# Kernel tuning notes

Measured on AMD Instinct MI355X. Metric: run time of the kernel, lower is better.

The kernel has to match this reference:

```python
import jax, jax.numpy as jnp
import numpy as np

N_ROIS = 10000
N_CLS = 151          # Visual Genome: 150 object classes + background
NMS_THRESH = 0.3     # filter_det default
SCORE_THRESH = 0.05  # ObjectDetector thresh
MAX_PER_IMG = 64     # ObjectDetector max_per_img
PRE_NMS_TOPN = 6000  # filter_det default
POST_NMS_TOPN = 300  # filter_det default


def setup_inputs() -> dict:
    key = jax.random.key(0)
    k1, k2, k3, k4, k5 = jax.random.split(key, 5)
    # class-probability-like scores (rows sum to 1, like the softmax output fed to filter_det)
    scores = jax.nn.softmax(jax.random.normal(k1, (N_ROIS, N_CLS)) * 2.0, axis=1)
    cx = jax.random.uniform(k2, (N_ROIS, N_CLS)) * 992.0
    cy = jax.random.uniform(k3, (N_ROIS, N_CLS)) * 992.0
    w = 4.0 + jax.random.uniform(k4, (N_ROIS, N_CLS)) * 156.0
    h = 4.0 + jax.random.uniform(k5, (N_ROIS, N_CLS)) * 156.0
    boxes = jnp.clip(jnp.stack([cx - w / 2, cy - h / 2, cx + w / 2, cy + h / 2], axis=-1), 0.0, 1023.0)
    return {"scores": scores.astype(jnp.float32), "boxes": boxes.astype(jnp.float32)}


def _nms_keep(scores_c, boxes_c):
    """apply_nms for one class: fixed-iteration greedy NMS -> bool keep mask [N]."""
    n = scores_c.shape[0]
    # pre_nms_topn: only the top-K scoring boxes are NMS candidates
    kth = jax.lax.top_k(scores_c, PRE_NMS_TOPN)[0][-1]
    active0 = scores_c >= kth
    keep0 = jnp.zeros((n,), dtype=bool)
    areas = (boxes_c[:, 2] - boxes_c[:, 0] + 1.0) * (boxes_c[:, 3] - boxes_c[:, 1] + 1.0)

    def step(carry, _):
        active, keep = carry
        s = jnp.where(active, scores_c, -jnp.inf)
        idx = jnp.argmax(s)
        valid = s[idx] > -jnp.inf  # any candidate left?
        keep = keep.at[idx].set(keep[idx] | valid)
        b = boxes_c[idx]
        ix1 = jnp.maximum(b[0], boxes_c[:, 0])
        iy1 = jnp.maximum(b[1], boxes_c[:, 1])
        ix2 = jnp.minimum(b[2], boxes_c[:, 2])
        iy2 = jnp.minimum(b[3], boxes_c[:, 3])
        inter = jnp.maximum(ix2 - ix1 + 1.0, 0.0) * jnp.maximum(iy2 - iy1 + 1.0, 0.0)
        iou = inter / (areas[idx] + areas - inter)
        # suppress iou > thresh (self box has iou 1, so it is removed too)
        active = active & (iou <= NMS_THRESH)
        return (active, keep), None

    (_, keep), _ = jax.lax.scan(step, (active0, keep0), None, length=POST_NMS_TOPN)
    return keep


def reference(scores, boxes):
    """filter_det: per-class NMS mask + cross-class dedupe + top max_per_img."""
    # per-class NMS, vmapped over the class axis -> keep mask [N, C]
    keep = jax.vmap(_nms_keep, in_axes=(1, 1), out_axes=1)(scores, boxes)
    keep = jax.lax.stop_gradient(keep)  # mask built from .data in the original
    # valid_cls: skip background (col 0) and classes whose best score <= thresh
    col_valid = (jnp.max(scores, axis=0) > SCORE_THRESH).at[0].set(False)
    nms_mask = keep & col_valid[None, :]
    dists_all = jnp.where(nms_mask, scores, 0.0)  # nms_mask * scores
    # nms_filter_duplicates: one label per box (argmax over classes)
    scores_pre = jnp.max(dists_all, axis=1)
    labels_pre = jnp.argmax(dists_all, axis=1)
    # sort descending, threshold, cap at max_per_img (fixed-shape top_k + validity mask)
    s_masked = jnp.where(scores_pre > SCORE_THRESH, scores_pre, -jnp.inf)
    top_v, top_i = jax.lax.top_k(s_masked, MAX_PER_IMG)
    valid = top_v > SCORE_THRESH
    top_scores = jnp.where(valid, top_v, 0.0)
    top_labels = jnp.where(valid, labels_pre[top_i], -1)
    top_inds = jnp.where(valid, top_i, -1)
    return dists_all, top_scores, top_inds, top_labels
```

## Files before the change

### kernel.cpp

```cpp
#include <hip/hip_runtime.h>

typedef unsigned long long u64;
typedef unsigned int u32;

#define N_ROIS   10000
#define N_CLS    151
#define PRE_TOPN 6000
#define POST_TOPN 300
#define MAX_PER  64
#define NMS_TH   0.3f
#define SCORE_TH 0.05f

#define BLOCKA   1024
#define NWAVES   (BLOCKA / 64)
#define BANDK    1024
#define BANDCAP  1536
#define CHUNK    512
#define CWORDS   (CHUNK / 32)
#define TROWS    10240

#define SBITS_OFF 0
#define KEYS_OFF  40000
#define RNK_OFF   52288
#define SBOX_OFF  58432
#define SIDX_OFF  83008
#define SUPP_OFF  89152
#define KBOX_OFF  121920
#define SMEM_BYTES 126784

__device__ __forceinline__ bool suppresses(float4 a, float4 b)
{
#pragma clang fp contract(off)
    float areaa = (a.z - a.x + 1.f) * (a.w - a.y + 1.f);
    float areab = (b.z - b.x + 1.f) * (b.w - b.y + 1.f);
    float ix1 = fmaxf(a.x, b.x), iy1 = fmaxf(a.y, b.y);
    float ix2 = fminf(a.z, b.z), iy2 = fminf(a.w, b.w);
    float iw = fmaxf(ix2 - ix1 + 1.f, 0.f);
    float ih = fmaxf(iy2 - iy1 + 1.f, 0.f);
    float inter = iw * ih;
    float iou = inter / (areaa + areab - inter);
    return iou > NMS_TH;
}

__global__ __launch_bounds__(BLOCKA)
void nms_kernel(const float* __restrict__ scores,
                const float* __restrict__ scoresT,
                const float* __restrict__ boxes,
                float* __restrict__ dists,
                u64* __restrict__ rowkey,
                int useT)
{
    extern __shared__ __align__(16) char smem[];
    __shared__ int s_cnts[32];
    __shared__ int s_cc, s_nk, s_chg;
    __shared__ u32 s_redu[NWAVES];
    __shared__ u32 s_alive[CWORDS], s_rz[CWORDS];
    __shared__ u32 s_K[CWORDS], s_Supp[CWORDS];
    __shared__ int s_wpre[CWORDS];
    __shared__ int s_wofs[NWAVES + 1];
    __shared__ int s_resume;

    u32*    sbits = (u32*)smem;
    u64*    keys  = (u64*)(smem + KEYS_OFF);
    u32*    rnk   = (u32*)(smem + RNK_OFF);
    float4* sbox  = (float4*)(smem + SBOX_OFF);
    u32*    sidx  = (u32*)(smem + SIDX_OFF);
    u32*    supp  = (u32*)(smem + SUPP_OFF);
    float4* kbox  = (float4*)(smem + KBOX_OFF);

    const int c    = blockIdx.x + 1;
    const int tid  = threadIdx.x;
    const int lane = tid & 63, wid = tid >> 6;

    u32 lmax = 0;
    if (useT) {
        const float* colp = scoresT + (size_t)c * TROWS;
        for (int r = tid; r < N_ROIS; r += BLOCKA) {
            u32 b = __float_as_uint(colp[r]); sbits[r] = b; lmax = b > lmax ? b : lmax;
        }
    } else {
        for (int r = tid; r < N_ROIS; r += BLOCKA) {
            u32 b = __float_as_uint(scores[(size_t)r * N_CLS + c]); sbits[r] = b; lmax = b > lmax ? b : lmax;
        }
    }
    for (int off = 32; off; off >>= 1) { u32 o = __shfl_down(lmax, off); lmax = o > lmax ? o : lmax; }
    if (lane == 0) s_redu[wid] = lmax;
    if (tid < 32) s_cnts[tid] = 0;
    __syncthreads();
    if (tid == 0) {
        u32 m = s_redu[0];
        for (int w = 1; w < NWAVES; ++w) m = s_redu[w] > m ? s_redu[w] : m;
        s_redu[0] = m; s_nk = 0;
    }
    __syncthreads();
    if (s_redu[0] <= __float_as_uint(SCORE_TH)) return;

    int slot = 0;
    auto count_ge = [&](u32 v) -> int {
        int cnt = 0;
        const u64* sb2 = (const u64*)sbits;
        for (int r2 = tid; r2 < N_ROIS / 2; r2 += BLOCKA) {
            u64 two = sb2[r2];
            cnt += ((u32)two >= v) ? 1 : 0;
            cnt += ((u32)(two >> 32) >= v) ? 1 : 0;
        }
        for (int off = 32; off; off >>= 1) cnt += __shfl_down(cnt, off);
        if (lane == 0 && cnt) atomicAdd(&s_cnts[slot & 31], cnt);
        __syncthreads();
        int total = s_cnts[slot & 31];
        if (tid == 0) s_cnts[(slot + 16) & 31] = 0;
        ++slot;
        return total;
    };

    auto compactRange = [&](u32 vlo, u32 vhiX, int pos0) -> int {
        if (tid == 0) s_cc = 0;
        __syncthreads();
        for (int r = tid; r < TROWS; r += BLOCKA) {
            bool pred = (r < N_ROIS) && (sbits[r] >= vlo) && (sbits[r] < vhiX);
            u64 ball = __ballot(pred);
            int bpos = 0, bcnt = __popcll(ball);
            if (lane == 0 && bcnt) bpos = atomicAdd(&s_cc, bcnt);
            bpos = __shfl(bpos, 0);
            if (pred) {
                int pos = pos0 + bpos + (int)__popcll(ball & ((1ull << lane) - 1ull));
                if (pos < BANDCAP)
                    keys[pos] = ((u64)sbits[r] << 32) | (u64)(0xFFFFFFFFu - (u32)r);
            }
        }
        __syncthreads();
        return s_cc;
    };

    auto emitEq = [&](u32 v, int rowStart, int pos0, int capN, int* emittedOut) -> int {
        int run = 0, resume = N_ROIS;
        for (int r0 = 0; r0 < N_ROIS; r0 += BLOCKA) {
            if (r0 + BLOCKA <= rowStart) continue;
            int r = r0 + tid;
            bool pred = (r < N_ROIS) && (r >= rowStart) && (sbits[r] == v);
            u64 ball = __ballot(pred);
            if (lane == 0) s_wofs[wid] = __popcll(ball);
            __syncthreads();
            if (tid == 0) {
                int acc = 0;
                for (int w = 0; w < NWAVES; ++w) { int cw = s_wofs[w]; s_wofs[w] = acc; acc += cw; }
                s_wofs[NWAVES] = acc; s_resume = N_ROIS;
            }
            __syncthreads();
            int tot = s_wofs[NWAVES];
            if (pred) {
                int idx = run + s_wofs[wid] + (int)__popcll(ball & ((1ull << lane) - 1ull));
                if (idx < capN) keys[pos0 + idx] = ((u64)v << 32) | (u64)(0xFFFFFFFFu - (u32)r);
                else atomicMin(&s_resume, r);
            }
            __syncthreads();
            if (run + tot > capN) {
                resume = s_resume < (r0 + BLOCKA) ? s_resume : (r0 + BLOCKA);
                run = capN;
                break;
            }
            run += tot;
        }
        *emittedOut = run;
        return resume;
    };

    u32 Vhi = 0x80000000u;
    int procCnt = 0, knum = 0;
    u32 Vfloor = 0; int eligTotal = 0x7FFFFFFF; bool haveFloor = false;
    u32 eqV = 0; int eqRow = N_ROIS; bool eqPend = false;

    for (int band = 0; band < 64 && knum < POST_TOPN; ++band) {
        int C = 0;
        if (eqPend) {
            int E; int resume = emitEq(eqV, eqRow, 0, BANDCAP, &E);
            C = E; procCnt += E;
            if (resume >= N_ROIS) { eqPend = false; Vhi = eqV; }
            eqRow = resume;
            if (C == 0) { if (eqPend) break; else continue; }
        } else {
            if (band >= 1) {
                if (!haveFloor) {
                    u32 V = 0; int cv = N_ROIS;
                    for (int b = 30; b >= 0; --b) {
                        u32 cd = V | (1u << b);
                        int c2 = count_ge(cd);
                        if (c2 >= PRE_TOPN) { V = cd; cv = c2; }
                    }
                    Vfloor = V; eligTotal = cv; haveFloor = true;
                }
                if (procCnt >= eligTotal) break;
            }
            int target = procCnt + BANDK;
            int capAbs = procCnt + BANDCAP;
            u32 V = 0; int cv = N_ROIS;
            for (int b = 30; b >= 16; --b) {
                u32 cd = V | (1u << b);
                int c2 = count_ge(cd);
                if (c2 >= target) { V = cd; cv = c2; }
            }
            for (int b = 15; b >= 0 && cv > capAbs; --b) {
                u32 cd = V | (1u << b);
                int c2 = count_ge(cd);
                if (c2 >= target) { V = cd; cv = c2; }
            }
            if (haveFloor && V < Vfloor) { V = Vfloor; cv = eligTotal; }
            if (cv > capAbs) {
                int ngt = compactRange(V + 1, Vhi, 0);
                int E; int resume = emitEq(V, 0, ngt, BANDCAP - ngt, &E);
                C = ngt + E; procCnt += C;
                eqV = V; eqRow = resume; eqPend = (resume < N_ROIS);
                if (!eqPend) Vhi = V;
            } else {
                C = compactRange(V, Vhi, 0);
                procCnt = cv; Vhi = V;
            }
            if (C <= 0) continue;
        }

        for (int q = tid; q < BANDCAP; q += BLOCKA) rnk[q] = 0;
        __syncthreads();
        {
            int q0 = tid >> 1, par = tid & 1;
            for (int q = q0; q < C; q += BLOCKA / 2) {
                u64 kq = keys[q]; int partial = 0;
                for (int p = par; p < C; p += 2) partial += (keys[p] > kq) ? 1 : 0;
                atomicAdd(&rnk[q], (u32)partial);
            }
        }
        __syncthreads();
        for (int q = tid; q < C; q += BLOCKA) {
            u64 kq = keys[q];
            u32 pos = rnk[q];
            u32 r = 0xFFFFFFFFu - (u32)kq;
            sidx[pos] = r;
            sbox[pos] = *(const float4*)(boxes + ((size_t)r * N_CLS + c) * 4);
        }
        __syncthreads();

        for (int base = 0; base < C && knum < POST_TOPN; base += CHUNK) {
            int chunkN = (C - base) < CHUNK ? (C - base) : CHUNK;
            int knum0 = knum;

            if (tid < CHUNK) {
                bool al = false;
                if (tid < chunkN) {
                    al = true;
                    float4 bq = sbox[base + tid];
                    for (int j = 0; j < knum0; ++j)
                        if (suppresses(kbox[j], bq)) { al = false; break; }
                }
                u64 ball = __ballot(al);
                if (lane == 0) { s_alive[wid * 2] = (u32)ball; s_alive[wid * 2 + 1] = (u32)(ball >> 32); }
            }
            if (tid < CWORDS) s_rz[tid] = 0;
            for (int w = tid; w < CHUNK * CWORDS; w += BLOCKA) supp[w] = 0;
            __syncthreads();

            {
                int q0 = tid >> 1, par = tid & 1;
                if (q0 < chunkN && ((s_alive[q0 >> 5] >> (q0 & 31)) & 1u)) {
                    float4 bq = sbox[base + q0];
                    for (int p = par; p < q0; p += 2) {
                        if (!((s_alive[p >> 5] >> (p & 31)) & 1u)) continue;
                        if (suppresses(sbox[base + p], bq)) {
                            atomicOr(&supp[(p << 4) + (q0 >> 5)], 1u << (q0 & 31));
                            atomicOr(&s_rz[p >> 5], 1u << (p & 31));
                        }
                    }
                }
            }
            if (tid < CWORDS) s_K[tid] = 0;
            __syncthreads();

            if (tid < CWORDS) s_K[tid] = s_alive[tid];
            for (;;) {
                __syncthreads();
                if (tid < CWORDS) s_Supp[tid] = 0;
                if (tid == 0) s_chg = 0;
                __syncthreads();
                for (int pw = tid; pw < (chunkN << 4); pw += BLOCKA) {
                    int p = pw >> 4, w = pw & 15;
                    if (((s_rz[p >> 5] >> (p & 31)) & 1u) &&
                        ((s_K[p >> 5] >> (p & 31)) & 1u)) {
                        u32 rw = supp[(p << 4) + w];
                        if (rw) atomicOr(&s_Supp[w], rw);
                    }
                }
                __syncthreads();
                if (tid < CWORDS) {
                    u32 nk = s_alive[tid] & ~s_Supp[tid];
                    if (nk != s_K[tid]) { s_K[tid] = nk; atomicOr(&s_chg, 1); }
                }
                __syncthreads();
                if (!s_chg) break;
            }

            if (wid == 0) {
                u32 kw = (lane < CWORDS) ? s_K[lane] : 0u;
                int pc = __popc(kw);
                int inc = pc;
                for (int off = 1; off < 32; off <<= 1) { int o = __shfl_up(inc, off); if (lane >= off) inc += o; }
                int ex = inc - pc;
                int budget = POST_TOPN - knum0;
                u32 fin = kw;
                if (ex >= budget) fin = 0;
                else {
                    int need = budget - ex;
                    if (pc > need) {
                        while (__popc(fin) > need) fin &= ~(1u << (31 - __clz(fin)));
                    }
                }
                int pc2 = __popc(fin);
                int inc2 = pc2;
                for (int off = 1; off < 32; off <<= 1) { int o = __shfl_up(inc2, off); if (lane >= off) inc2 += o; }
                if (lane < CWORDS) { s_K[lane] = fin; s_wpre[lane] = inc2 - pc2; }
                if (lane == CWORDS - 1) s_nk = knum0 + inc2;
            }
            __syncthreads();

            if (tid < CHUNK) {
                int w = tid >> 5, b = tid & 31;
                u32 word = s_K[w];
                if ((word >> b) & 1u) {
                    int rank = knum0 + s_wpre[w] + __popc(word & ((1u << b) - 1u));
                    int q = base + tid;
                    u32 r = sidx[q];
                    u32 sb = sbits[r];
                    kbox[rank] = sbox[q];
                    dists[(size_t)r * N_CLS + c] = __uint_as_float(sb);
                    atomicMax(rowkey + r, ((u64)sb << 32) | (u64)(0xFFFFFFFFu - (u32)c));
                }
            }
            __syncthreads();
            knum = s_nk;
        }
    }
}

__global__ __launch_bounds__(1024)
void transpose_zero_kernel(const float* __restrict__ in, float* __restrict__ outT,
                           float* __restrict__ dists, u64* __restrict__ rowkey, int useT)
{
    __shared__ float tile[32][33];
    if (useT) {
        int tx = threadIdx.x & 31, ty = threadIdx.x >> 5;
        int rb = blockIdx.x * 32, cb = blockIdx.y * 32;
        int r = rb + ty, cc = cb + tx;
        tile[ty][tx] = (r < N_ROIS && cc < N_CLS) ? in[(size_t)r * N_CLS + cc] : 0.f;
        __syncthreads();
        int oc = cb + ty, orr = rb + tx;
        if (oc < N_CLS) outT[(size_t)oc * TROWS + orr] = tile[tx][ty];
    }
    int bid = blockIdx.y * gridDim.x + blockIdx.x;
    int flat = bid * 1024 + threadIdx.x;
    if (flat < N_ROIS * N_CLS) dists[flat] = 0.f;
    if (flat < N_ROIS) rowkey[flat] = 0ull;
}

__global__ __launch_bounds__(BLOCKA)
void topk_kernel(const u64* __restrict__ rowkey, float* __restrict__ out)
{
    __shared__ u32 shi[N_ROIS];
    __shared__ int s_cnts[32];
    __shared__ int s_cc;
    __shared__ u64 cand[192];
    __shared__ int s_wofs[NWAVES + 1];
    const int tid = threadIdx.x, lane = tid & 63, wid = tid >> 6;

    if (tid < 32) s_cnts[tid] = 0;
    if (tid == 0) s_cc = 0;
    if (tid < 192) cand[tid] = 0;
    for (int i = tid; i < N_ROIS; i += BLOCKA) {
        u64 rk = rowkey[i];
        u32 hb = (u32)(rk >> 32);
        shi[i] = (__uint_as_float(hb) > SCORE_TH) ? hb : 0u;
    }
    __syncthreads();

    int slot = 0;
    auto count_ge = [&](u32 v) -> int {
        int cnt = 0;
        const u64* s2 = (const u64*)shi;
        for (int r2 = tid; r2 < N_ROIS / 2; r2 += BLOCKA) {
            u64 two = s2[r2];
            cnt += ((u32)two >= v) ? 1 : 0;
            cnt += ((u32)(two >> 32) >= v) ? 1 : 0;
        }
        for (int off = 32; off; off >>= 1) cnt += __shfl_down(cnt, off);
        if (lane == 0 && cnt) atomicAdd(&s_cnts[slot & 31], cnt);
        __syncthreads();
        int total = s_cnts[slot & 31];
        if (tid == 0) s_cnts[(slot + 16) & 31] = 0;
        ++slot;
        return total;
    };

    const int cap = 128;
    u32 V = 0; int cv = N_ROIS;
    for (int b = 30; b >= 16; --b) {
        u32 cd = V | (1u << b);
        int c2 = count_ge(cd);
        if (c2 >= MAX_PER) { V = cd; cv = c2; }
    }
    for (int b = 15; b >= 0 && cv > cap; --b) {
        u32 cd = V | (1u << b);
        int c2 = count_ge(cd);
        if (c2 >= MAX_PER) { V = cd; cv = c2; }
    }
    if (V == 0) { V = 1; cv = count_ge(1); }
    int C = 0;
    if (cv > cap) {
        if (tid == 0) s_cc = 0;
        __syncthreads();
        for (int i = tid; i < TROWS; i += BLOCKA) {
            bool pred = (i < N_ROIS) && (shi[i] >= V + 1);
            u64 ball = __ballot(pred);
            int bpos = 0, bcnt = __popcll(ball);
            if (lane == 0 && bcnt) bpos = atomicAdd(&s_cc, bcnt);
            bpos = __shfl(bpos, 0);
            if (pred) {
                int pos = bpos + (int)__popcll(ball & ((1ull << lane) - 1ull));
                if (pos < cap) cand[pos] = ((u64)shi[i] << 32) | (u64)(0xFFFFFFFFu - (u32)i);
            }
        }
        __syncthreads();
        int ngt = s_cc; if (ngt > cap) ngt = cap;
        int need = MAX_PER - ngt;
        int run = 0;
        for (int r0 = 0; r0 < N_ROIS && run < need; r0 += BLOCKA) {
            int r = r0 + tid;
            bool pred = (r < N_ROIS) && (shi[r] == V);
            u64 ball = __ballot(pred);
            if (lane == 0) s_wofs[wid] = __popcll(ball);
            __syncthreads();
            if (tid == 0) {
                int acc = 0;
                for (int w = 0; w < NWAVES; ++w) { int cw = s_wofs[w]; s_wofs[w] = acc; acc += cw; }
                s_wofs[NWAVES] = acc;
            }
            __syncthreads();
            int tot = s_wofs[NWAVES];
            if (pred) {
                int idx = run + s_wofs[wid] + (int)__popcll(ball & ((1ull << lane) - 1ull));
                if (idx < need) cand[ngt + idx] = ((u64)V << 32) | (u64)(0xFFFFFFFFu - (u32)r);
            }
            __syncthreads();
            run += tot;
        }
        C = ngt + (run < need ? run : need);
    } else {
        if (tid == 0) s_cc = 0;
        __syncthreads();
        for (int i = tid; i < TROWS; i += BLOCKA) {
            bool pred = (i < N_ROIS) && (shi[i] >= V);
            u64 ball = __ballot(pred);
            int bpos = 0, bcnt = __popcll(ball);
            if (lane == 0 && bcnt) bpos = atomicAdd(&s_cc, bcnt);
            bpos = __shfl(bpos, 0);
            if (pred) {
                int pos = bpos + (int)__popcll(ball & ((1ull << lane) - 1ull));
                if (pos < cap) cand[pos] = ((u64)shi[i] << 32) | (u64)(0xFFFFFFFFu - (u32)i);
            }
        }
        __syncthreads();
        C = s_cc; if (C > cap) C = cap;
    }

    float* out_s = out + (size_t)N_ROIS * N_CLS;
    float* out_i = out_s + MAX_PER;
    float* out_l = out_i + MAX_PER;

    int myrank = -1; u64 myk = 0;
    if (tid < C) {
        myk = cand[tid];
        myrank = 0;
        for (int p = 0; p < C; ++p) myrank += (cand[p] > myk) ? 1 : 0;
    }
    if (tid < MAX_PER) { out_s[tid] = 0.f; out_i[tid] = -1.f; out_l[tid] = -1.f; }
    __syncthreads();
    if (tid < C && myrank < MAX_PER) {
        u32 r = 0xFFFFFFFFu - (u32)myk;
        out_s[myrank] = __uint_as_float((u32)(myk >> 32));
        out_i[myrank] = (float)r;
        out_l[myrank] = (float)(0xFFFFFFFFu - (u32)rowkey[r]);
    }
}

extern "C" void kernel_launch(void* const* d_in, const int* in_sizes, int n_in,
                              void* d_out, int out_size, void* d_ws, size_t ws_size,
                              hipStream_t stream)
{
    const float* scores = (const float*)d_in[0];
    const float* boxes  = (const float*)d_in[1];
    float* out = (float*)d_out;
    u64* rowkey = (u64*)d_ws;

    size_t needT = 80000 + (size_t)N_CLS * TROWS * sizeof(float);
    int useT = (ws_size >= needT) ? 1 : 0;
    float* scoresT = (float*)((char*)d_ws + 80000);

    (void)hipFuncSetAttribute((const void*)nms_kernel,
                              hipFuncAttributeMaxDynamicSharedMemorySize, SMEM_BYTES);

    transpose_zero_kernel<<<dim3(320, 5), 1024, 0, stream>>>(scores, scoresT, out, rowkey, useT);
    nms_kernel<<<N_CLS - 1, BLOCKA, SMEM_BYTES, stream>>>(scores, scoresT, boxes, out, rowkey, useT);
    topk_kernel<<<1, BLOCKA, 0, stream>>>(rowkey, out);
}
```

Baseline: 259.2 us.

## Split per-class NMS into histogram-based selection and greedy kernels

Splits the monolithic per-class NMS kernel into a select kernel and a greedy kernel. The select kernel builds a 1024-bin histogram with cumulative counts, which replaces most of the bitwise radix-search count passes when choosing the first band threshold. The greedy kernel reuses the saved cumulative histogram for later bands and checks candidates against already-kept boxes in parallel. It also raises the band size and cap. This adds an extra kernel launch, workspace traffic for selected rows, headers and histograms, and a larger O(C²) rank sort per band.

```diff
diff --git a/kernel.cpp b/kernel.cpp
--- a/kernel.cpp
+++ b/kernel.cpp
@@ -2,6 +2,7 @@
 
 typedef unsigned long long u64;
 typedef unsigned int u32;
+typedef unsigned short u16;
 
 #define N_ROIS   10000
 #define N_CLS    151
@@ -12,21 +13,34 @@
 #define SCORE_TH 0.05f
 
 #define BLOCKA   1024
-#define NWAVES   (BLOCKA / 64)
-#define BANDK    1024
-#define BANDCAP  1536
+#define NWAVES   16
+#define BANDK    1536
+#define BANDCAP  2048
 #define CHUNK    512
-#define CWORDS   (CHUNK / 32)
+#define CWORDS   16
 #define TROWS    10240
-
-#define SBITS_OFF 0
-#define KEYS_OFF  40000
-#define RNK_OFF   52288
-#define SBOX_OFF  58432
-#define SIDX_OFF  83008
-#define SUPP_OFF  89152
-#define KBOX_OFF  121920
-#define SMEM_BYTES 126784
+#define NBINS    1024
+
+#define WS_SROWS 80000
+#define WS_HDR   694400
+#define WS_CUM   699200
+#define WS_SCT   1313600
+#define WS_NEED  7498560
+
+#define S_HIST_OFF 40000
+#define S_KEYS_OFF 44096
+#define S_RNK_OFF  60480
+#define S_SMEM     68672
+
+#define G_SIDX_OFF  32768
+#define G_SSC_OFF   40960
+#define G_SUPP_OFF  49152
+#define G_KEYS2_OFF 49152
+#define G_RNK2_OFF  65536
+#define G_KBOX_OFF  81920
+#define G_CUM_OFF   86784
+#define G_SBITS_OFF 90880
+#define G_SMEM      130880
 
 __device__ __forceinline__ bool suppresses(float4 a, float4 b)
 {
@@ -43,62 +57,66 @@
 }
 
 __global__ __launch_bounds__(BLOCKA)
-void nms_kernel(const float* __restrict__ scores,
-                const float* __restrict__ scoresT,
-                const float* __restrict__ boxes,
-                float* __restrict__ dists,
-                u64* __restrict__ rowkey,
-                int useT)
+void select_kernel(const float* __restrict__ scores, const float* __restrict__ scoresT,
+                   u16* __restrict__ srows, u32* __restrict__ hdr, u32* __restrict__ cumg,
+                   int useT)
 {
     extern __shared__ __align__(16) char smem[];
     __shared__ int s_cnts[32];
-    __shared__ int s_cc, s_nk, s_chg;
+    __shared__ int s_cc, s_sel, s_resume;
     __shared__ u32 s_redu[NWAVES];
-    __shared__ u32 s_alive[CWORDS], s_rz[CWORDS];
-    __shared__ u32 s_K[CWORDS], s_Supp[CWORDS];
-    __shared__ int s_wpre[CWORDS];
     __shared__ int s_wofs[NWAVES + 1];
-    __shared__ int s_resume;
-
-    u32*    sbits = (u32*)smem;
-    u64*    keys  = (u64*)(smem + KEYS_OFF);
-    u32*    rnk   = (u32*)(smem + RNK_OFF);
-    float4* sbox  = (float4*)(smem + SBOX_OFF);
-    u32*    sidx  = (u32*)(smem + SIDX_OFF);
-    u32*    supp  = (u32*)(smem + SUPP_OFF);
-    float4* kbox  = (float4*)(smem + KBOX_OFF);
-
-    const int c    = blockIdx.x + 1;
-    const int tid  = threadIdx.x;
-    const int lane = tid & 63, wid = tid >> 6;
+
+    u32* sbits = (u32*)smem;
+    u32* hist  = (u32*)(smem + S_HIST_OFF);
+    u64* keys  = (u64*)(smem + S_KEYS_OFF);
+    u32* rnk   = (u32*)(smem + S_RNK_OFF);
+
+    const int c = blockIdx.x + 1, tid = threadIdx.x, lane = tid & 63, wid = tid >> 6;
+    u32* myhdr = hdr + (size_t)blockIdx.x * 8;
 
     u32 lmax = 0;
     if (useT) {
         const float* colp = scoresT + (size_t)c * TROWS;
-        for (int r = tid; r < N_ROIS; r += BLOCKA) {
-            u32 b = __float_as_uint(colp[r]); sbits[r] = b; lmax = b > lmax ? b : lmax;
-        }
+        for (int r = tid; r < N_ROIS; r += BLOCKA) { u32 b = __float_as_uint(colp[r]); sbits[r] = b; lmax = b > lmax ? b : lmax; }
     } else {
-        for (int r = tid; r < N_ROIS; r += BLOCKA) {
-            u32 b = __float_as_uint(scores[(size_t)r * N_CLS + c]); sbits[r] = b; lmax = b > lmax ? b : lmax;
-        }
+        for (int r = tid; r < N_ROIS; r += BLOCKA) { u32 b = __float_as_uint(scores[(size_t)r * N_CLS + c]); sbits[r] = b; lmax = b > lmax ? b : lmax; }
     }
     for (int off = 32; off; off >>= 1) { u32 o = __shfl_down(lmax, off); lmax = o > lmax ? o : lmax; }
     if (lane == 0) s_redu[wid] = lmax;
     if (tid < 32) s_cnts[tid] = 0;
-    __syncthreads();
-    if (tid == 0) {
-        u32 m = s_redu[0];
-        for (int w = 1; w < NWAVES; ++w) m = s_redu[w] > m ? s_redu[w] : m;
-        s_redu[0] = m; s_nk = 0;
-    }
-    __syncthreads();
-    if (s_redu[0] <= __float_as_uint(SCORE_TH)) return;
+    if (tid == 0) s_sel = 0;
+    for (int b = tid; b < NBINS; b += BLOCKA) hist[b] = 0;
+    __syncthreads();
+    if (tid == 0) { u32 m = s_redu[0]; for (int w = 1; w < NWAVES; ++w) m = s_redu[w] > m ? s_redu[w] : m; s_redu[0] = m; }
+    __syncthreads();
+    if (s_redu[0] <= __float_as_uint(SCORE_TH)) { if (tid == 0) myhdr[0] = 0; return; }
+
+    for (int r = tid; r < N_ROIS; r += BLOCKA) atomicAdd(&hist[sbits[r] >> 21], 1u);
+    __syncthreads();
+    {
+        u32* A = hist; u32* Bb = rnk;
+        for (int off = 1; off < NBINS; off <<= 1) {
+            if (tid < NBINS) Bb[tid] = A[tid] + ((tid + off < NBINS) ? A[tid + off] : 0u);
+            __syncthreads();
+            u32* t = A; A = Bb; Bb = t;
+        }
+        if (A != hist) { if (tid < NBINS) hist[tid] = A[tid]; __syncthreads(); }
+    }
+    if (tid < NBINS) cumg[(size_t)blockIdx.x * NBINS + tid] = hist[tid];
+
+    {
+        bool pred = (tid < NBINS) && (hist[tid] >= (u32)BANDK);
+        u64 ball = __ballot(pred);
+        if (lane == 0 && ball) atomicAdd(&s_sel, (int)__popcll(ball));
+    }
+    __syncthreads();
+    int B0 = s_sel - 1;
+    u32 V = (u32)B0 << 21; int cv = (int)hist[B0];
 
     int slot = 0;
     auto count_ge = [&](u32 v) -> int {
-        int cnt = 0;
-        const u64* sb2 = (const u64*)sbits;
+        int cnt = 0; const u64* sb2 = (const u64*)sbits;
         for (int r2 = tid; r2 < N_ROIS / 2; r2 += BLOCKA) {
             u64 two = sb2[r2];
             cnt += ((u32)two >= v) ? 1 : 0;
@@ -109,10 +127,8 @@
         __syncthreads();
         int total = s_cnts[slot & 31];
         if (tid == 0) s_cnts[(slot + 16) & 31] = 0;
-        ++slot;
-        return total;
+        ++slot; return total;
     };
-
     auto compactRange = [&](u32 vlo, u32 vhiX, int pos0) -> int {
         if (tid == 0) s_cc = 0;
         __syncthreads();
@@ -124,14 +140,11 @@
             bpos = __shfl(bpos, 0);
             if (pred) {
                 int pos = pos0 + bpos + (int)__popcll(ball & ((1ull << lane) - 1ull));
-                if (pos < BANDCAP)
-                    keys[pos] = ((u64)sbits[r] << 32) | (u64)(0xFFFFFFFFu - (u32)r);
-            }
-        }
-        __syncthreads();
-        return s_cc;
+                if (pos < BANDCAP) keys[pos] = ((u64)sbits[r] << 32) | (u64)(0xFFFFFFFFu - (u32)r);
+            }
+        }
+        __syncthreads(); return s_cc;
     };
-
     auto emitEq = [&](u32 v, int rowStart, int pos0, int capN, int* emittedOut) -> int {
         int run = 0, resume = N_ROIS;
         for (int r0 = 0; r0 < N_ROIS; r0 += BLOCKA) {
@@ -156,133 +169,144 @@
             __syncthreads();
             if (run + tot > capN) {
                 resume = s_resume < (r0 + BLOCKA) ? s_resume : (r0 + BLOCKA);
-                run = capN;
-                break;
+                run = capN; break;
             }
             run += tot;
         }
-        *emittedOut = run;
-        return resume;
+        *emittedOut = run; return resume;
     };
 
-    u32 Vhi = 0x80000000u;
-    int procCnt = 0, knum = 0;
-    u32 Vfloor = 0; int eligTotal = 0x7FFFFFFF; bool haveFloor = false;
-    u32 eqV = 0; int eqRow = N_ROIS; bool eqPend = false;
-
-    for (int band = 0; band < 64 && knum < POST_TOPN; ++band) {
-        int C = 0;
-        if (eqPend) {
-            int E; int resume = emitEq(eqV, eqRow, 0, BANDCAP, &E);
-            C = E; procCnt += E;
-            if (resume >= N_ROIS) { eqPend = false; Vhi = eqV; }
-            eqRow = resume;
-            if (C == 0) { if (eqPend) break; else continue; }
-        } else {
-            if (band >= 1) {
-                if (!haveFloor) {
-                    u32 V = 0; int cv = N_ROIS;
-                    for (int b = 30; b >= 0; --b) {
-                        u32 cd = V | (1u << b);
-                        int c2 = count_ge(cd);
-                        if (c2 >= PRE_TOPN) { V = cd; cv = c2; }
-                    }
-                    Vfloor = V; eligTotal = cv; haveFloor = true;
-                }
-                if (procCnt >= eligTotal) break;
-            }
-            int target = procCnt + BANDK;
-            int capAbs = procCnt + BANDCAP;
-            u32 V = 0; int cv = N_ROIS;
-            for (int b = 30; b >= 16; --b) {
-                u32 cd = V | (1u << b);
-                int c2 = count_ge(cd);
-                if (c2 >= target) { V = cd; cv = c2; }
-            }
-            for (int b = 15; b >= 0 && cv > capAbs; --b) {
-                u32 cd = V | (1u << b);
-                int c2 = count_ge(cd);
-                if (c2 >= target) { V = cd; cv = c2; }
-            }
-            if (haveFloor && V < Vfloor) { V = Vfloor; cv = eligTotal; }
-            if (cv > capAbs) {
-                int ngt = compactRange(V + 1, Vhi, 0);
-                int E; int resume = emitEq(V, 0, ngt, BANDCAP - ngt, &E);
-                C = ngt + E; procCnt += C;
-                eqV = V; eqRow = resume; eqPend = (resume < N_ROIS);
-                if (!eqPend) Vhi = V;
-            } else {
-                C = compactRange(V, Vhi, 0);
-                procCnt = cv; Vhi = V;
-            }
-            if (C <= 0) continue;
-        }
-
-        for (int q = tid; q < BANDCAP; q += BLOCKA) rnk[q] = 0;
-        __syncthreads();
-        {
-            int q0 = tid >> 1, par = tid & 1;
-            for (int q = q0; q < C; q += BLOCKA / 2) {
-                u64 kq = keys[q]; int partial = 0;
-                for (int p = par; p < C; p += 2) partial += (keys[p] > kq) ? 1 : 0;
-                atomicAdd(&rnk[q], (u32)partial);
-            }
-        }
-        __syncthreads();
-        for (int q = tid; q < C; q += BLOCKA) {
-            u64 kq = keys[q];
-            u32 pos = rnk[q];
-            u32 r = 0xFFFFFFFFu - (u32)kq;
-            sidx[pos] = r;
-            sbox[pos] = *(const float4*)(boxes + ((size_t)r * N_CLS + c) * 4);
-        }
-        __syncthreads();
-
-        for (int base = 0; base < C && knum < POST_TOPN; base += CHUNK) {
-            int chunkN = (C - base) < CHUNK ? (C - base) : CHUNK;
+    for (int b = 20; b >= 0 && cv > BANDCAP; --b) {
+        u32 cd = V | (1u << b);
+        int c2 = count_ge(cd);
+        if (c2 >= BANDK) { V = cd; cv = c2; }
+    }
+
+    int C, procCnt, eqPend = 0, eqRow = N_ROIS; u32 Vhi = 0x80000000u, eqV = 0;
+    if (cv > BANDCAP) {
+        int ngt = compactRange(V + 1, 0x80000000u, 0);
+        int E; int resume = emitEq(V, 0, ngt, BANDCAP - ngt, &E);
+        C = ngt + E; procCnt = C; eqV = V; eqRow = resume; eqPend = (resume < N_ROIS) ? 1 : 0;
+        if (!eqPend) Vhi = V;
+    } else {
+        C = compactRange(V, 0x80000000u, 0);
+        procCnt = cv; Vhi = V;
+    }
+
+    for (int q = tid; q < BANDCAP; q += BLOCKA) rnk[q] = 0;
+    __syncthreads();
+    {
+        int q0 = tid >> 1, par = tid & 1;
+        for (int q = q0; q < C; q += BLOCKA / 2) {
+            u64 kq = keys[q]; int partial = 0;
+            for (int p = par; p < C; p += 2) partial += (keys[p] > kq) ? 1 : 0;
+            atomicAdd(&rnk[q], (u32)partial);
+        }
+    }
+    __syncthreads();
+    for (int q = tid; q < C; q += BLOCKA) {
+        u32 r = 0xFFFFFFFFu - (u32)keys[q];
+        srows[(size_t)blockIdx.x * BANDCAP + rnk[q]] = (u16)r;
+    }
+    if (tid == 0) {
+        myhdr[0] = 1; myhdr[1] = (u32)C; myhdr[2] = (u32)procCnt; myhdr[3] = Vhi;
+        myhdr[4] = (u32)eqPend; myhdr[5] = eqV; myhdr[6] = (u32)eqRow; myhdr[7] = 0;
+    }
+}
+
+__global__ __launch_bounds__(BLOCKA)
+void greedy_kernel(const float* __restrict__ scores, const float* __restrict__ scoresT,
+                   const float* __restrict__ boxes,
+                   const u16* __restrict__ srows, const u32* __restrict__ hdr,
+                   const u32* __restrict__ cumg,
+                   float* __restrict__ dists, u64* __restrict__ rowkey, int useT)
+{
+    extern __shared__ __align__(16) char smem[];
+    __shared__ int s_cnts[32];
+    __shared__ int s_cc, s_nk, s_chg, s_sel, s_resume;
+    __shared__ u32 s_hd[8];
+    __shared__ u32 s_alive[CWORDS], s_rz[CWORDS], s_K[CWORDS], s_Supp[CWORDS];
+    __shared__ int s_wpre[CWORDS];
+    __shared__ int s_wofs[NWAVES + 1];
+
+    float4* sbox  = (float4*)smem;
+    u32*    sidx  = (u32*)(smem + G_SIDX_OFF);
+    u32*    ssc   = (u32*)(smem + G_SSC_OFF);
+    u32*    supp  = (u32*)(smem + G_SUPP_OFF);
+    u64*    keys2 = (u64*)(smem + G_KEYS2_OFF);
+    u32*    rnk2  = (u32*)(smem + G_RNK2_OFF);
+    float4* kbox  = (float4*)(smem + G_KBOX_OFF);
+    u32*    cum   = (u32*)(smem + G_CUM_OFF);
+    u32*    sbits = (u32*)(smem + G_SBITS_OFF);
+
+    const int c = blockIdx.x + 1, tid = threadIdx.x, lane = tid & 63, wid = tid >> 6;
+
+    if (tid < 8) s_hd[tid] = hdr[(size_t)blockIdx.x * 8 + tid];
+    if (tid < 32) s_cnts[tid] = 0;
+    if (tid == 0) s_nk = 0;
+    if (useT) {
+        const float* colp = scoresT + (size_t)c * TROWS;
+        for (int r = tid; r < N_ROIS; r += BLOCKA) sbits[r] = __float_as_uint(colp[r]);
+    } else {
+        for (int r = tid; r < N_ROIS; r += BLOCKA) sbits[r] = __float_as_uint(scores[(size_t)r * N_CLS + c]);
+    }
+    if (tid < NBINS) cum[tid] = cumg[(size_t)blockIdx.x * NBINS + tid];
+    __syncthreads();
+    if (!s_hd[0]) return;
+    int C = (int)s_hd[1];
+
+    for (int i = tid; i < C; i += BLOCKA) {
+        u32 r = (u32)srows[(size_t)blockIdx.x * BANDCAP + i];
+        sidx[i] = r; ssc[i] = sbits[r];
+        sbox[i] = *(const float4*)(boxes + ((size_t)r * N_CLS + c) * 4);
+    }
+    __syncthreads();
+
+    auto runGreedy = [&](int Cb, int knumIn) -> int {
+        int knum = knumIn;
+        for (int base = 0; base < Cb && knum < POST_TOPN; base += CHUNK) {
+            int chunkN = (Cb - base) < CHUNK ? (Cb - base) : CHUNK;
             int knum0 = knum;
-
-            if (tid < CHUNK) {
-                bool al = false;
-                if (tid < chunkN) {
-                    al = true;
-                    float4 bq = sbox[base + tid];
-                    for (int j = 0; j < knum0; ++j)
-                        if (suppresses(kbox[j], bq)) { al = false; break; }
-                }
-                u64 ball = __ballot(al);
-                if (lane == 0) { s_alive[wid * 2] = (u32)ball; s_alive[wid * 2 + 1] = (u32)(ball >> 32); }
-            }
-            if (tid < CWORDS) s_rz[tid] = 0;
-            for (int w = tid; w < CHUNK * CWORDS; w += BLOCKA) supp[w] = 0;
-            __syncthreads();
-
+            if (tid < CWORDS) {
+                int rem = chunkN - tid * 32;
+                s_alive[tid] = (rem <= 0) ? 0u : ((rem >= 32) ? 0xFFFFFFFFu : ((1u << rem) - 1u));
+                s_rz[tid] = 0u;
+            }
+            for (int w = tid; w < CHUNK * CWORDS; w += BLOCKA) supp[w] = 0u;
+            __syncthreads();
+            if (knum0 > 0) {
+                int cand = tid >> 1, half = tid & 1;
+                if (cand < chunkN) {
+                    float4 bq = sbox[base + cand];
+                    for (int j = half; j < knum0; j += 2)
+                        if (suppresses(kbox[j], bq)) { atomicAnd(&s_alive[cand >> 5], ~(1u << (cand & 31))); break; }
+                }
+                __syncthreads();
+            }
             {
                 int q0 = tid >> 1, par = tid & 1;
-                if (q0 < chunkN && ((s_alive[q0 >> 5] >> (q0 & 31)) & 1u)) {
-                    float4 bq = sbox[base + q0];
-                    for (int p = par; p < q0; p += 2) {
+                for (int q = q0; q < chunkN; q += BLOCKA / 2) {
+                    if (!((s_alive[q >> 5] >> (q & 31)) & 1u)) continue;
+                    float4 bq = sbox[base + q];
+                    for (int p = par; p < q; p += 2) {
                         if (!((s_alive[p >> 5] >> (p & 31)) & 1u)) continue;
                         if (suppresses(sbox[base + p], bq)) {
-                            atomicOr(&supp[(p << 4) + (q0 >> 5)], 1u << (q0 & 31));
+                            atomicOr(&supp[(p << 4) + (q >> 5)], 1u << (q & 31));
                             atomicOr(&s_rz[p >> 5], 1u << (p & 31));
                         }
                     }
                 }
             }
-            if (tid < CWORDS) s_K[tid] = 0;
-            __syncthreads();
-
+            __syncthreads();
             if (tid < CWORDS) s_K[tid] = s_alive[tid];
             for (;;) {
                 __syncthreads();
-                if (tid < CWORDS) s_Supp[tid] = 0;
+                if (tid < CWORDS) s_Supp[tid] = 0u;
                 if (tid == 0) s_chg = 0;
                 __syncthreads();
                 for (int pw = tid; pw < (chunkN << 4); pw += BLOCKA) {
                     int p = pw >> 4, w = pw & 15;
-                    if (((s_rz[p >> 5] >> (p & 31)) & 1u) &&
-                        ((s_K[p >> 5] >> (p & 31)) & 1u)) {
+                    if (((s_rz[p >> 5] >> (p & 31)) & 1u) && ((s_K[p >> 5] >> (p & 31)) & 1u)) {
                         u32 rw = supp[(p << 4) + w];
                         if (rw) atomicOr(&s_Supp[w], rw);
                     }
@@ -295,7 +319,6 @@
                 __syncthreads();
                 if (!s_chg) break;
             }
-
             if (wid == 0) {
                 u32 kw = (lane < CWORDS) ? s_K[lane] : 0u;
                 int pc = __popc(kw);
@@ -307,9 +330,7 @@
                 if (ex >= budget) fin = 0;
                 else {
                     int need = budget - ex;
-                    if (pc > need) {
-                        while (__popc(fin) > need) fin &= ~(1u << (31 - __clz(fin)));
-                    }
+                    if (pc > need) { while (__popc(fin) > need) fin &= ~(1u << (31 - __clz(fin))); }
                 }
                 int pc2 = __popc(fin);
                 int inc2 = pc2;
@@ -318,15 +339,13 @@
                 if (lane == CWORDS - 1) s_nk = knum0 + inc2;
             }
             __syncthreads();
-
             if (tid < CHUNK) {
                 int w = tid >> 5, b = tid & 31;
                 u32 word = s_K[w];
                 if ((word >> b) & 1u) {
                     int rank = knum0 + s_wpre[w] + __popc(word & ((1u << b) - 1u));
                     int q = base + tid;
-                    u32 r = sidx[q];
-                    u32 sb = sbits[r];
+                    u32 r = sidx[q], sb = ssc[q];
                     kbox[rank] = sbox[q];
                     dists[(size_t)r * N_CLS + c] = __uint_as_float(sb);
                     atomicMax(rowkey + r, ((u64)sb << 32) | (u64)(0xFFFFFFFFu - (u32)c));
@@ -334,6 +353,144 @@
             }
             __syncthreads();
             knum = s_nk;
+        }
+        return knum;
+    };
+
+    int knum = runGreedy(C, 0);
+
+    if (knum < POST_TOPN) {
+        int procCnt = (int)s_hd[2]; u32 Vhi = s_hd[3];
+        int eqPend = (int)s_hd[4]; u32 eqV = s_hd[5]; int eqRow = (int)s_hd[6];
+        bool haveFloor = false; u32 Vfloor = 0; int eligTotal = 0x7FFFFFFF;
+        int slot = 0;
+        auto count_ge = [&](u32 v) -> int {
+            int cnt = 0; const u64* sb2 = (const u64*)sbits;
+            for (int r2 = tid; r2 < N_ROIS / 2; r2 += BLOCKA) {
+                u64 two = sb2[r2];
+                cnt += ((u32)two >= v) ? 1 : 0;
+                cnt += ((u32)(two >> 32) >= v) ? 1 : 0;
+            }
+            for (int off = 32; off; off >>= 1) cnt += __shfl_down(cnt, off);
+            if (lane == 0 && cnt) atomicAdd(&s_cnts[slot & 31], cnt);
+            __syncthreads();
+            int total = s_cnts[slot & 31];
+            if (tid == 0) s_cnts[(slot + 16) & 31] = 0;
+            ++slot; return total;
+        };
+        auto compactRange = [&](u32 vlo, u32 vhiX, int pos0) -> int {
+            if (tid == 0) s_cc = 0;
+            __syncthreads();
+            for (int r = tid; r < TROWS; r += BLOCKA) {
+                bool pred = (r < N_ROIS) && (sbits[r] >= vlo) && (sbits[r] < vhiX);
+                u64 ball = __ballot(pred);
+                int bpos = 0, bcnt = __popcll(ball);
+                if (lane == 0 && bcnt) bpos = atomicAdd(&s_cc, bcnt);
+                bpos = __shfl(bpos, 0);
+                if (pred) {
+                    int pos = pos0 + bpos + (int)__popcll(ball & ((1ull << lane) - 1ull));
+                    if (pos < BANDCAP) keys2[pos] = ((u64)sbits[r] << 32) | (u64)(0xFFFFFFFFu - (u32)r);
+                }
+            }
+            __syncthreads(); return s_cc;
+        };
+        auto emitEq = [&](u32 v, int rowStart, int pos0, int capN, int* emittedOut) -> int {
+            int run = 0, resume = N_ROIS;
+            for (int r0 = 0; r0 < N_ROIS; r0 += BLOCKA) {
+                if (r0 + BLOCKA <= rowStart) continue;
+                int r = r0 + tid;
+                bool pred = (r < N_ROIS) && (r >= rowStart) && (sbits[r] == v);
+                u64 ball = __ballot(pred);
+                if (lane == 0) s_wofs[wid] = __popcll(ball);
+                __syncthreads();
+                if (tid == 0) {
+                    int acc = 0;
+                    for (int w = 0; w < NWAVES; ++w) { int cw = s_wofs[w]; s_wofs[w] = acc; acc += cw; }
+                    s_wofs[NWAVES] = acc; s_resume = N_ROIS;
+                }
+                __syncthreads();
+                int tot = s_wofs[NWAVES];
+                if (pred) {
+                    int idx = run + s_wofs[wid] + (int)__popcll(ball & ((1ull << lane) - 1ull));
+                    if (idx < capN) keys2[pos0 + idx] = ((u64)v << 32) | (u64)(0xFFFFFFFFu - (u32)r);
+                    else atomicMin(&s_resume, r);
+                }
+                __syncthreads();
+                if (run + tot > capN) {
+                    resume = s_resume < (r0 + BLOCKA) ? s_resume : (r0 + BLOCKA);
+                    run = capN; break;
+                }
+                run += tot;
+            }
+            *emittedOut = run; return resume;
+        };
+
+        for (int band = 0; band < 64 && knum < POST_TOPN; ++band) {
+            int Cb = 0;
+            if (eqPend) {
+                int E; int resume = emitEq(eqV, eqRow, 0, BANDCAP, &E);
+                Cb = E; procCnt += E;
+                if (resume >= N_ROIS) { eqPend = 0; Vhi = eqV; }
+                eqRow = resume;
+                if (Cb == 0) { if (eqPend) break; else continue; }
+            } else {
+                if (!haveFloor) {
+                    u32 Vf = 0; int cvf = N_ROIS;
+                    for (int b = 30; b >= 0; --b) {
+                        u32 cd = Vf | (1u << b);
+                        int c2 = count_ge(cd);
+                        if (c2 >= PRE_TOPN) { Vf = cd; cvf = c2; }
+                    }
+                    Vfloor = Vf; eligTotal = cvf; haveFloor = true;
+                }
+                if (procCnt >= eligTotal) break;
+                int target = procCnt + BANDK, capAbs = procCnt + BANDCAP;
+                if (tid == 0) s_sel = 0;
+                __syncthreads();
+                {
+                    bool pred = (tid < NBINS) && (cum[tid] >= (u32)target);
+                    u64 ball = __ballot(pred);
+                    if (lane == 0 && ball) atomicAdd(&s_sel, (int)__popcll(ball));
+                }
+                __syncthreads();
+                int nb = s_sel;
+                u32 V; int cv2;
+                if (nb <= 0) { V = 0u; cv2 = (int)cum[0]; }
+                else { V = (u32)(nb - 1) << 21; cv2 = (int)cum[nb - 1]; }
+                for (int b = 20; b >= 0 && cv2 > capAbs; --b) {
+                    u32 cd = V | (1u << b);
+                    int c2 = count_ge(cd);
+                    if (c2 >= target) { V = cd; cv2 = c2; }
+                }
+                if (haveFloor && V < Vfloor) { V = Vfloor; cv2 = eligTotal; }
+                if (cv2 > capAbs) {
+                    int ngt = compactRange(V + 1, Vhi, 0);
+                    int E; int resume = emitEq(V, 0, ngt, BANDCAP - ngt, &E);
+                    Cb = ngt + E; procCnt += Cb; eqV = V; eqRow = resume; eqPend = (resume < N_ROIS) ? 1 : 0;
+                    if (!eqPend) Vhi = V;
+                } else {
+                    Cb = compactRange(V, Vhi, 0); procCnt = cv2; Vhi = V;
+                }
+                if (Cb <= 0) continue;
+            }
+            for (int q = tid; q < BANDCAP; q += BLOCKA) rnk2[q] = 0;
+            __syncthreads();
+            {
+                int q0 = tid >> 1, par = tid & 1;
+                for (int q = q0; q < Cb; q += BLOCKA / 2) {
+                    u64 kq = keys2[q]; int partial = 0;
+                    for (int p = par; p < Cb; p += 2) partial += (keys2[p] > kq) ? 1 : 0;
+                    atomicAdd(&rnk2[q], (u32)partial);
+                }
+            }
+            __syncthreads();
+            for (int q = tid; q < Cb; q += BLOCKA) {
+                u64 kq = keys2[q]; u32 pos = rnk2[q]; u32 r = 0xFFFFFFFFu - (u32)kq;
+                sidx[pos] = r; ssc[pos] = (u32)(kq >> 32);
+                sbox[pos] = *(const float4*)(boxes + ((size_t)r * N_CLS + c) * 4);
+            }
+            __syncthreads();
+            knum = runGreedy(Cb, knum);
         }
     }
 }
@@ -380,8 +537,7 @@
 
     int slot = 0;
     auto count_ge = [&](u32 v) -> int {
-        int cnt = 0;
-        const u64* s2 = (const u64*)shi;
+        int cnt = 0; const u64* s2 = (const u64*)shi;
         for (int r2 = tid; r2 < N_ROIS / 2; r2 += BLOCKA) {
             u64 two = s2[r2];
             cnt += ((u32)two >= v) ? 1 : 0;
@@ -392,8 +548,7 @@
         __syncthreads();
         int total = s_cnts[slot & 31];
         if (tid == 0) s_cnts[(slot + 16) & 31] = 0;
-        ++slot;
-        return total;
+        ++slot; return total;
     };
 
     const int cap = 128;
@@ -494,16 +649,21 @@
     const float* scores = (const float*)d_in[0];
     const float* boxes  = (const float*)d_in[1];
     float* out = (float*)d_out;
-    u64* rowkey = (u64*)d_ws;
-
-    size_t needT = 80000 + (size_t)N_CLS * TROWS * sizeof(float);
-    int useT = (ws_size >= needT) ? 1 : 0;
-    float* scoresT = (float*)((char*)d_ws + 80000);
-
-    (void)hipFuncSetAttribute((const void*)nms_kernel,
-                              hipFuncAttributeMaxDynamicSharedMemorySize, SMEM_BYTES);
+
+    u64* rowkey  = (u64*)d_ws;
+    u16* srows   = (u16*)((char*)d_ws + WS_SROWS);
+    u32* hdr     = (u32*)((char*)d_ws + WS_HDR);
+    u32* cumg    = (u32*)((char*)d_ws + WS_CUM);
+    float* scoresT = (float*)((char*)d_ws + WS_SCT);
+    int useT = (ws_size >= (size_t)WS_NEED) ? 1 : 0;
+
+    (void)hipFuncSetAttribute((const void*)select_kernel,
+                              hipFuncAttributeMaxDynamicSharedMemorySize, S_SMEM);
+    (void)hipFuncSetAttribute((const void*)greedy_kernel,
+                              hipFuncAttributeMaxDynamicSharedMemorySize, G_SMEM);
 
     transpose_zero_kernel<<<dim3(320, 5), 1024, 0, stream>>>(scores, scoresT, out, rowkey, useT);
-    nms_kernel<<<N_CLS - 1, BLOCKA, SMEM_BYTES, stream>>>(scores, scoresT, boxes, out, rowkey, useT);
+    select_kernel<<<N_CLS - 1, BLOCKA, S_SMEM, stream>>>(scores, scoresT, srows, hdr, cumg, useT);
+    greedy_kernel<<<N_CLS - 1, BLOCKA, G_SMEM, stream>>>(scores, scoresT, boxes, srows, hdr, cumg, out, rowkey, useT);
     topk_kernel<<<1, BLOCKA, 0, stream>>>(rowkey, out);
 }
```

Result: slower. 344.0 us (+32.7%).
